# Kernel tuning notes

Hardware: AMD Instinct MI355X
Metric: run time of the kernel (lower is better)

## Reference

```python
import jax, jax.numpy as jnp
import numpy as np
import math

L, D, H, PK, N = 3, 512, 8, 8, 3072
DK = D // H


def _layernorm(x, s, b):
    m = jnp.mean(x, axis=-1, keepdims=True)
    v = jnp.mean((x - m) ** 2, axis=-1, keepdims=True)
    return (x - m) / jnp.sqrt(v + 1e-6) * s + b


def setup_inputs() -> dict:
    key = jax.random.key(0)
    ks = jax.random.split(key, 12)
    p = lambda k, shape: jax.random.normal(k, shape, jnp.float32) * (1.0 / math.sqrt(shape[-1]))
    x = jax.random.normal(ks[0], (N, D), jnp.float32)
    adm = jax.random.randint(ks[1], (N, N), 0, PK, jnp.int32)
    return {
        "x": x,
        "adm": adm,
        "ln_att_s": jnp.ones((L, D), jnp.float32),
        "ln_att_b": jnp.zeros((L, D), jnp.float32),
        "Wq": p(ks[2], (L, D, D)),
        "Wk": p(ks[3], (L, D, D)),
        "Wv": p(ks[4], (L, D, D)),
        "rel_k": p(ks[5], (L, PK, DK)),
        "Wg": p(ks[6], (L, D, D)) * 0.0,  # gating weight init to 0 in original
        "bg": jnp.ones((L, D), jnp.float32),  # gating bias init to 1
        "Wo": p(ks[7], (L, D, D)),
        "bo": jnp.zeros((L, D), jnp.float32),
        "ln_ff_s": jnp.ones((L, D), jnp.float32),
        "ln_ff_b": jnp.zeros((L, D), jnp.float32),
        "W1": p(ks[8], (L, D, 2 * D)),
        "b1": jnp.zeros((L, 2 * D), jnp.float32),
        "W2": p(ks[9], (L, 2 * D, D)),
        "b2": jnp.zeros((L, D), jnp.float32),
    }


def reference(x, adm, ln_att_s, ln_att_b, Wq, Wk, Wv, rel_k, Wg, bg, Wo, bo,
              ln_ff_s, ln_ff_b, W1, b1, W2, b2):
    att_scores = []
    idx = jnp.broadcast_to(adm[None], (H, N, N))  # one_hot(gpm) @ r  ==  gather r along PK
    for n in range(L):
        xn = _layernorm(x, ln_att_s[n], ln_att_b[n])  # same layer_norm applied to x_q and x_k
        q = (xn @ Wq[n]).reshape(N, H, DK).transpose(1, 0, 2)  # [H,N,DK]
        k = (xn @ Wk[n]).reshape(N, H, DK).transpose(1, 0, 2)
        v = (xn @ Wv[n]).reshape(N, H, DK).transpose(1, 0, 2)
        attn1 = jnp.einsum('hid,hjd->hij', q, k)  # [H,N,N]
        rq = jnp.einsum('hid,pd->hip', q, rel_k[n])  # [H,N,PK]
        attn2 = jnp.take_along_axis(rq, idx, axis=2)  # [H,N,N]
        attn = jax.nn.softmax((attn1 + attn2) / math.sqrt(DK), axis=-1)
        out = jnp.einsum('hij,hjd->hid', attn, v).transpose(1, 0, 2).reshape(N, D)
        gate = jax.nn.sigmoid(xn @ Wg[n] + bg[n])
        m = (out * gate) @ Wo[n] + bo[n]
        # FFN with pre-layernorm, residual: x = x + pff(x + m)
        y = x + m
        yn = _layernorm(y, ln_ff_s[n], ln_ff_b[n])
        ff = jax.nn.gelu(yn @ W1[n] + b1[n], approximate=True) @ W2[n] + b2[n]
        x = x + ff
        att_scores.append(attn)
    return (x, jnp.stack(att_scores))
```

## Files before the change

kernel.cpp:

```cpp
#include <hip/hip_runtime.h>
#include <math.h>

#define NT 3072
#define DIM 512
#define NH 8
#define DKH 64
#define PKN 8
#define D2 1024
#define NL 3

typedef float4 f4;
typedef unsigned short ushort_t;
typedef unsigned char uchar_t;
typedef __attribute__((ext_vector_type(8))) short s8x;
typedef __attribute__((ext_vector_type(4))) float fx4;

#define MFMA(a, b, c) __builtin_amdgcn_mfma_f32_16x16x32_bf16(a, b, c, 0, 0, 0)

__device__ __forceinline__ float b2f(ushort_t u) {
  union { unsigned int x; float f; } c;
  c.x = (unsigned int)u << 16;
  return c.f;
}
__device__ __forceinline__ ushort_t f2b(float f) {
  union { float f; unsigned int x; } c;
  c.f = f;
  unsigned int r = (c.x + 0x7FFFu + ((c.x >> 16) & 1u)) >> 16;
  return (ushort_t)r;
}

__device__ __forceinline__ float wred_sum(float v) {
#pragma unroll
  for (int off = 32; off > 0; off >>= 1) v += __shfl_xor(v, off);
  return v;
}

__global__ __launch_bounds__(256) void ln_bf16_kernel(
    const float* __restrict__ x, const float* __restrict__ s,
    const float* __restrict__ b, ushort_t* __restrict__ out) {
  int row = blockIdx.x;
  const float* xr = x + (size_t)row * DIM;
  int t = threadIdx.x;
  float v0 = xr[t], v1 = xr[t + 256];
  float sum = wred_sum(v0 + v1);
  float sq = wred_sum(v0 * v0 + v1 * v1);
  __shared__ float ss[4], s2[4];
  if ((t & 63) == 0) { ss[t >> 6] = sum; s2[t >> 6] = sq; }
  __syncthreads();
  float tot = ss[0] + ss[1] + ss[2] + ss[3];
  float tot2 = s2[0] + s2[1] + s2[2] + s2[3];
  float mean = tot * (1.0f / DIM);
  float var = tot2 * (1.0f / DIM) - mean * mean;
  float inv = rsqrtf(var + 1e-6f);
  ushort_t* orow = out + (size_t)row * DIM;
  orow[t] = f2b((v0 - mean) * inv * s[t] + b[t]);
  orow[t + 256] = f2b((v1 - mean) * inv * s[t + 256] + b[t + 256]);
}

__global__ __launch_bounds__(256) void tconv_kernel(const float* __restrict__ W,
                                                    ushort_t* __restrict__ Wt,
                                                    int K, int Nc) {
  __shared__ float Ls[64][65];
  int t = threadIdx.x;
  int n0 = blockIdx.x * 64, k0 = blockIdx.y * 64;
  int rr = t >> 4, cc = (t & 15) * 4;
#pragma unroll
  for (int p = 0; p < 4; ++p) {
    f4 v = *(const f4*)&W[(size_t)(k0 + rr + p * 16) * Nc + n0 + cc];
    Ls[rr + p * 16][cc + 0] = v.x;
    Ls[rr + p * 16][cc + 1] = v.y;
    Ls[rr + p * 16][cc + 2] = v.z;
    Ls[rr + p * 16][cc + 3] = v.w;
  }
  __syncthreads();
  int nr = t >> 2, kc = (t & 3) * 16;
  ushort_t tmp[16];
#pragma unroll
  for (int e = 0; e < 16; ++e) tmp[e] = f2b(Ls[kc + e][nr]);
  ushort_t* dst = &Wt[(size_t)(n0 + nr) * K + k0 + kc];
  *(uint4*)dst = *(uint4*)&tmp[0];
  *(uint4*)(dst + 8) = *(uint4*)&tmp[8];
}

__global__ __launch_bounds__(256) void adm8_kernel(const int* __restrict__ adm,
                                                   uchar_t* __restrict__ out) {
  size_t i = ((size_t)blockIdx.x * 256 + threadIdx.x) * 4;
  int4 v = *(const int4*)&adm[i];
  unsigned int b = (unsigned)(v.x & 255) | ((unsigned)(v.y & 255) << 8) |
                   ((unsigned)(v.z & 255) << 16) | ((unsigned)(v.w & 255) << 24);
  *(unsigned int*)&out[i] = b;
}

__global__ __launch_bounds__(64) void rq_kernel(const ushort_t* __restrict__ q,
                                                const float* __restrict__ relk,
                                                float* __restrict__ rq) {
  int i = blockIdx.x;
  int t = threadIdx.x;
  int h = t >> 3, p = t & 7;
  const ushort_t* qi = q + (size_t)i * DIM + h * DKH;
  const float* rp = relk + p * DKH;
  float s = 0.f;
#pragma unroll
  for (int d = 0; d < DKH; ++d) s = fmaf(b2f(qi[d]), rp[d], s);
  rq[(size_t)i * 64 + h * 8 + p] = s;
}

template <int ACT, bool OBF>
__global__ __launch_bounds__(256) void gemm_bf16(
    const ushort_t* __restrict__ A, const ushort_t* __restrict__ mul,
    const ushort_t* __restrict__ Bt, const float* __restrict__ bias,
    const float* __restrict__ res, void* __restrict__ Cp, int K, int ldc,
    float scale) {
  __shared__ __align__(16) ushort_t As[2048];
  __shared__ __align__(16) ushort_t Bs[2048];
  int t = threadIdx.x;
  int i0 = blockIdx.y * 64, j0 = blockIdx.x * 64;
  int w = t >> 6, l = t & 63;
  int wm = w >> 1, wn = w & 1;
  int lr = l >> 4, lc = l & 15;
  int fo = lr * 16 + (lc ^ (lr << 2));
  int am = t >> 2, akg = t & 3;
  int aoff = ((am >> 4) * 4 + akg) * 16 + ((am & 15) ^ (akg << 2));
  const ushort_t* Aptr = A + (size_t)(i0 + am) * K + akg * 8;
  const ushort_t* Mptr = mul ? mul + (size_t)(i0 + am) * K + akg * 8 : nullptr;
  int bc = l, bkg = w;
  int boff = ((bc >> 4) * 4 + bkg) * 16 + ((bc & 15) ^ (bkg << 2));
  const ushort_t* Bptr = Bt + (size_t)(j0 + bc) * K + bkg * 8;

  fx4 acc[2][2] = {};
  for (int k0 = 0; k0 < K; k0 += 32) {
    uint4 a = *(const uint4*)(Aptr + k0);
    if (mul) {
      uint4 m = *(const uint4*)(Mptr + k0);
      ushort_t* ap = (ushort_t*)&a;
      const ushort_t* mp = (const ushort_t*)&m;
#pragma unroll
      for (int e = 0; e < 8; ++e) ap[e] = f2b(b2f(ap[e]) * b2f(mp[e]));
    }
    *(uint4*)&As[aoff * 8] = a;
    *(uint4*)&Bs[boff * 8] = *(const uint4*)(Bptr + k0);
    __syncthreads();
    s8x a0 = *(const s8x*)&As[((wm * 2 + 0) * 64 + fo) * 8];
    s8x a1 = *(const s8x*)&As[((wm * 2 + 1) * 64 + fo) * 8];
    s8x b0 = *(const s8x*)&Bs[((wn * 2 + 0) * 64 + fo) * 8];
    s8x b1 = *(const s8x*)&Bs[((wn * 2 + 1) * 64 + fo) * 8];
    acc[0][0] = MFMA(a0, b0, acc[0][0]);
    acc[0][1] = MFMA(a0, b1, acc[0][1]);
    acc[1][0] = MFMA(a1, b0, acc[1][0]);
    acc[1][1] = MFMA(a1, b1, acc[1][1]);
    __syncthreads();
  }
#pragma unroll
  for (int ms = 0; ms < 2; ++ms) {
#pragma unroll
    for (int ns = 0; ns < 2; ++ns) {
#pragma unroll
      for (int r = 0; r < 4; ++r) {
        int i = i0 + (wm * 2 + ms) * 16 + lr * 4 + r;
        int j = j0 + (wn * 2 + ns) * 16 + lc;
        float o = acc[ms][ns][r] * scale;
        if (bias) o += bias[j];
        if (ACT == 1) {
          o = 1.0f / (1.0f + __expf(-o));
        } else if (ACT == 2) {
          float xx = o;
          float c = 0.7978845608028654f * (xx + 0.044715f * xx * xx * xx);
          o = 0.5f * xx * (1.0f + tanhf(c));
        }
        if (res) o += res[(size_t)i * ldc + j];
        if (OBF)
          ((ushort_t*)Cp)[(size_t)i * ldc + j] = f2b(o);
        else
          ((float*)Cp)[(size_t)i * ldc + j] = o;
      }
    }
  }
}

__global__ __launch_bounds__(256) void attn_kernel(
    const ushort_t* __restrict__ qb, const ushort_t* __restrict__ kb,
    const ushort_t* __restrict__ vb, const float* __restrict__ rqb,
    const uchar_t* __restrict__ adm8, float* __restrict__ att,
    ushort_t* __restrict__ av) {
  int h = blockIdx.y;
  int i0 = blockIdx.x * 64;
  __shared__ __align__(16) ushort_t Qs[4096];
  __shared__ __align__(16) ushort_t Ks[4096];
  __shared__ __align__(16) ushort_t Vs[4096];
  __shared__ __align__(16) ushort_t Ps[4096];
  __shared__ __align__(16) uchar_t adms[4096];
  __shared__ float rqs[64][8];
  int t = threadIdx.x, w = t >> 6, l = t & 63;
  int lr = l >> 4, lc = l & 15;
  int fo = lr * 16 + (lc ^ (lr << 2));
  {
    int am = t >> 2, akg = t & 3;
    int aoff = ((am >> 4) * 4 + akg) * 16 + ((am & 15) ^ (akg << 2));
    const ushort_t* qp = qb + (size_t)(i0 + am) * DIM + h * DKH + akg * 8;
    *(uint4*)&Qs[aoff * 8] = *(const uint4*)qp;
    *(uint4*)&Qs[2048 + aoff * 8] = *(const uint4*)(qp + 32);
  }
  if (t < 64) {
    const float* rp = &rqb[(size_t)(i0 + t) * 64 + h * 8];
    *(f4*)&rqs[t][0] = *(const f4*)rp;
    *(f4*)&rqs[t][4] = *(const f4*)(rp + 4);
  }
  __syncthreads();
  s8x qa0 = *(const s8x*)&Qs[(w * 64 + fo) * 8];
  s8x qa1 = *(const s8x*)&Qs[2048 + (w * 64 + fo) * 8];
  int bc = l, bkg = w;
  int boff = ((bc >> 4) * 4 + bkg) * 16 + ((bc & 15) ^ (bkg << 2));

  float m_run[4] = {-1e30f, -1e30f, -1e30f, -1e30f};
  float l_run[4] = {0.f, 0.f, 0.f, 0.f};

  for (int j0 = 0; j0 < NT; j0 += 64) {
    __syncthreads();
    const ushort_t* kp = kb + (size_t)(j0 + bc) * DIM + h * DKH + bkg * 8;
    *(uint4*)&Ks[boff * 8] = *(const uint4*)kp;
    *(uint4*)&Ks[2048 + boff * 8] = *(const uint4*)(kp + 32);
    *(uint4*)&adms[(t >> 2) * 64 + (t & 3) * 16] =
        *(const uint4*)&adm8[(size_t)(i0 + (t >> 2)) * NT + j0 + (t & 3) * 16];
    __syncthreads();
    fx4 sacc[4] = {};
#pragma unroll
    for (int nb = 0; nb < 4; ++nb) {
      s8x k0f = *(const s8x*)&Ks[(nb * 64 + fo) * 8];
      s8x k1f = *(const s8x*)&Ks[2048 + (nb * 64 + fo) * 8];
      sacc[nb] = MFMA(qa0, k0f, sacc[nb]);
      sacc[nb] = MFMA(qa1, k1f, sacc[nb]);
    }
#pragma unroll
    for (int r = 0; r < 4; ++r) {
      int il = w * 16 + lr * 4 + r;
      float sv[4];
      float tm = -1e30f;
#pragma unroll
      for (int nb = 0; nb < 4; ++nb) {
        sv[nb] = sacc[nb][r] + rqs[il][adms[il * 64 + nb * 16 + lc]];
        tm = fmaxf(tm, sv[nb]);
      }
      tm = fmaxf(tm, __shfl_xor(tm, 1));
      tm = fmaxf(tm, __shfl_xor(tm, 2));
      tm = fmaxf(tm, __shfl_xor(tm, 4));
      tm = fmaxf(tm, __shfl_xor(tm, 8));
      float mn = fmaxf(m_run[r], tm);
      float ssum = 0.f;
#pragma unroll
      for (int nb = 0; nb < 4; ++nb) ssum += __expf(sv[nb] - mn);
      ssum += __shfl_xor(ssum, 1);
      ssum += __shfl_xor(ssum, 2);
      ssum += __shfl_xor(ssum, 4);
      ssum += __shfl_xor(ssum, 8);
      l_run[r] = l_run[r] * __expf(m_run[r] - mn) + ssum;
      m_run[r] = mn;
    }
  }
  float linv[4];
#pragma unroll
  for (int r = 0; r < 4; ++r) linv[r] = 1.0f / l_run[r];

  fx4 oacc[4] = {};
  float* attb = att + ((size_t)h * NT + i0) * NT;
  for (int j0 = 0; j0 < NT; j0 += 64) {
    __syncthreads();
    const ushort_t* kp = kb + (size_t)(j0 + bc) * DIM + h * DKH + bkg * 8;
    *(uint4*)&Ks[boff * 8] = *(const uint4*)kp;
    *(uint4*)&Ks[2048 + boff * 8] = *(const uint4*)(kp + 32);
    *(uint4*)&adms[(t >> 2) * 64 + (t & 3) * 16] =
        *(const uint4*)&adm8[(size_t)(i0 + (t >> 2)) * NT + j0 + (t & 3) * 16];
#pragma unroll
    for (int cpass = 0; cpass < 2; ++cpass) {
      int cid = t + cpass * 256;
      int vks = cid >> 8, rem = cid & 255;
      int nb = rem >> 6, kg = (rem >> 4) & 3, s = rem & 15;
      const ushort_t* vp =
          vb + (size_t)(j0 + vks * 32 + kg * 8) * DIM + h * DKH + nb * 16 + s;
      ushort_t tmp[8];
#pragma unroll
      for (int e = 0; e < 8; ++e) tmp[e] = vp[(size_t)e * DIM];
      *(uint4*)&Vs[vks * 2048 + ((nb * 4 + kg) * 16 + (s ^ (kg << 2))) * 8] =
          *(uint4*)tmp;
    }
    __syncthreads();
    fx4 sacc[4] = {};
#pragma unroll
    for (int nb = 0; nb < 4; ++nb) {
      s8x k0f = *(const s8x*)&Ks[(nb * 64 + fo) * 8];
      s8x k1f = *(const s8x*)&Ks[2048 + (nb * 64 + fo) * 8];
      sacc[nb] = MFMA(qa0, k0f, sacc[nb]);
      sacc[nb] = MFMA(qa1, k1f, sacc[nb]);
    }
#pragma unroll
    for (int r = 0; r < 4; ++r) {
      int il = w * 16 + lr * 4 + r;
      int ir = il & 15;
#pragma unroll
      for (int nb = 0; nb < 4; ++nb) {
        int jl = nb * 16 + lc;
        float sval = sacc[nb][r] + rqs[il][adms[il * 64 + jl]];
        float p = __expf(sval - m_run[r]) * linv[r];
        attb[(size_t)il * NT + j0 + jl] = p;
        int pks = jl >> 5, pkg = (jl >> 3) & 3, pe = jl & 7;
        Ps[pks * 2048 + ((w * 4 + pkg) * 16 + (ir ^ (pkg << 2))) * 8 + pe] =
            f2b(p);
      }
    }
    __syncthreads();
#pragma unroll
    for (int ks = 0; ks < 2; ++ks) {
      s8x pa = *(const s8x*)&Ps[ks * 2048 + (w * 64 + fo) * 8];
#pragma unroll
      for (int nb = 0; nb < 4; ++nb) {
        s8x vf = *(const s8x*)&Vs[ks * 2048 + (nb * 64 + fo) * 8];
        oacc[nb] = MFMA(pa, vf, oacc[nb]);
      }
    }
  }
#pragma unroll
  for (int nb = 0; nb < 4; ++nb)
#pragma unroll
    for (int r = 0; r < 4; ++r)
      av[(size_t)(i0 + w * 16 + lr * 4 + r) * DIM + h * DKH + nb * 16 + lc] =
          f2b(oacc[nb][r]);
}

extern "C" void kernel_launch(void* const* d_in, const int* in_sizes, int n_in,
                              void* d_out, int out_size, void* d_ws,
                              size_t ws_size, hipStream_t stream) {
  const float* x_in = (const float*)d_in[0];
  const int* adm = (const int*)d_in[1];
  const float* ln_att_s = (const float*)d_in[2];
  const float* ln_att_b = (const float*)d_in[3];
  const float* Wq = (const float*)d_in[4];
  const float* Wk = (const float*)d_in[5];
  const float* Wv = (const float*)d_in[6];
  const float* rel_k = (const float*)d_in[7];
  const float* Wg = (const float*)d_in[8];
  const float* bg = (const float*)d_in[9];
  const float* Wo = (const float*)d_in[10];
  const float* bo = (const float*)d_in[11];
  const float* ln_ff_s = (const float*)d_in[12];
  const float* ln_ff_b = (const float*)d_in[13];
  const float* W1 = (const float*)d_in[14];
  const float* b1 = (const float*)d_in[15];
  const float* W2 = (const float*)d_in[16];
  const float* b2 = (const float*)d_in[17];
  float* out = (float*)d_out;

  const size_t ND = (size_t)NT * DIM;
  char* ws = (char*)d_ws;
  float* x_cur = (float*)ws;
  float* y = (float*)(ws + 6291456);
  ushort_t* qb = (ushort_t*)(ws + 12582912);
  ushort_t* kb = (ushort_t*)(ws + 15728640);
  ushort_t* vb = (ushort_t*)(ws + 18874368);
  ushort_t* gt = (ushort_t*)(ws + 22020096);
  ushort_t* avb = (ushort_t*)(ws + 25165824);
  ushort_t* xnb = (ushort_t*)(ws + 28311552);
  float* rqb = (float*)(ws + 31457280);
  uchar_t* adm8 = (uchar_t*)(ws + 32243712);
  ushort_t* Wt = (ushort_t*)(ws + 41680896);
  ushort_t* h1b = qb;

  ushort_t* Wtq = Wt;
  ushort_t* Wtk = Wt + 262144;
  ushort_t* Wtv = Wt + 524288;
  ushort_t* Wtg = Wt + 786432;
  ushort_t* Wto = Wt + 1048576;
  ushort_t* Wt1 = Wt + 1310720;
  ushort_t* Wt2 = Wt + 1835008;

  hipMemcpyAsync(x_cur, x_in, ND * sizeof(float), hipMemcpyDeviceToDevice,
                 stream);
  adm8_kernel<<<(NT * NT) / 1024, 256, 0, stream>>>(adm, adm8);

  dim3 gA(DIM / 64, NT / 64);
  dim3 gF1(D2 / 64, NT / 64);
  dim3 gT(8, 8);
  dim3 gT1(16, 8);
  dim3 gT2(8, 16);

  for (int n = 0; n < NL; ++n) {
    float* att = out + ND + (size_t)n * NH * NT * NT;
    size_t wo = (size_t)n * DIM * DIM;

    tconv_kernel<<<gT, 256, 0, stream>>>(Wq + wo, Wtq, DIM, DIM);
    tconv_kernel<<<gT, 256, 0, stream>>>(Wk + wo, Wtk, DIM, DIM);
    tconv_kernel<<<gT, 256, 0, stream>>>(Wv + wo, Wtv, DIM, DIM);
    tconv_kernel<<<gT, 256, 0, stream>>>(Wg + wo, Wtg, DIM, DIM);
    tconv_kernel<<<gT, 256, 0, stream>>>(Wo + wo, Wto, DIM, DIM);
    tconv_kernel<<<gT1, 256, 0, stream>>>(W1 + (size_t)n * DIM * D2, Wt1, DIM,
                                          D2);
    tconv_kernel<<<gT2, 256, 0, stream>>>(W2 + (size_t)n * D2 * DIM, Wt2, D2,
                                          DIM);

    ln_bf16_kernel<<<NT, 256, 0, stream>>>(x_cur, ln_att_s + n * DIM,
                                           ln_att_b + n * DIM, xnb);
    gemm_bf16<0, true><<<gA, 256, 0, stream>>>(xnb, nullptr, Wtq, nullptr,
                                               nullptr, qb, DIM, DIM, 0.125f);
    gemm_bf16<0, true><<<gA, 256, 0, stream>>>(xnb, nullptr, Wtk, nullptr,
                                               nullptr, kb, DIM, DIM, 1.0f);
    gemm_bf16<0, true><<<gA, 256, 0, stream>>>(xnb, nullptr, Wtv, nullptr,
                                               nullptr, vb, DIM, DIM, 1.0f);
    gemm_bf16<1, true><<<gA, 256, 0, stream>>>(xnb, nullptr, Wtg, bg + n * DIM,
                                               nullptr, gt, DIM, DIM, 1.0f);
    rq_kernel<<<NT, 64, 0, stream>>>(qb, rel_k + n * PKN * DKH, rqb);
    attn_kernel<<<dim3(NT / 64, NH), 256, 0, stream>>>(qb, kb, vb, rqb, adm8,
                                                       att, avb);
    gemm_bf16<0, false><<<gA, 256, 0, stream>>>(avb, gt, Wto, bo + n * DIM,
                                                x_cur, y, DIM, DIM, 1.0f);
    ln_bf16_kernel<<<NT, 256, 0, stream>>>(y, ln_ff_s + n * DIM,
                                           ln_ff_b + n * DIM, xnb);
    gemm_bf16<2, true><<<gF1, 256, 0, stream>>>(xnb, nullptr, Wt1, b1 + n * D2,
                                                nullptr, h1b, DIM, D2, 1.0f);
    gemm_bf16<0, false><<<gA, 256, 0, stream>>>(h1b, nullptr, Wt2, b2 + n * DIM,
                                                x_cur, x_cur, D2, DIM, 1.0f);
  }
  hipMemcpyAsync(out, x_cur, ND * sizeof(float), hipMemcpyDeviceToDevice,
                 stream);
}
```

Before: 1.199 ms.

## Fuse QKVG projections, restructure attention with split-KV waves and async LDS loads

```diff
diff --git a/kernel.cpp b/kernel.cpp
--- a/kernel.cpp
+++ b/kernel.cpp
@@ -8,6 +8,7 @@
 #define PKN 8
 #define D2 1024
 #define NL 3
+#define QS 2048
 
 typedef float4 f4;
 typedef unsigned short ushort_t;
@@ -16,6 +17,7 @@
 typedef __attribute__((ext_vector_type(4))) float fx4;
 
 #define MFMA(a, b, c) __builtin_amdgcn_mfma_f32_16x16x32_bf16(a, b, c, 0, 0, 0)
+#define EX2(x) __builtin_amdgcn_exp2f(x)
 
 __device__ __forceinline__ float b2f(ushort_t u) {
   union { unsigned int x; float f; } c;
@@ -28,11 +30,15 @@
   unsigned int r = (c.x + 0x7FFFu + ((c.x >> 16) & 1u)) >> 16;
   return (ushort_t)r;
 }
-
 __device__ __forceinline__ float wred_sum(float v) {
 #pragma unroll
   for (int off = 32; off > 0; off >>= 1) v += __shfl_xor(v, off);
   return v;
+}
+__device__ __forceinline__ void gload16(const ushort_t* g, ushort_t* l) {
+  __builtin_amdgcn_global_load_lds(
+      (const __attribute__((address_space(1))) unsigned int*)(const void*)g,
+      (__attribute__((address_space(3))) unsigned int*)(void*)l, 16, 0, 0);
 }
 
 __global__ __launch_bounds__(256) void ln_bf16_kernel(
@@ -57,12 +63,12 @@
   orow[t + 256] = f2b((v1 - mean) * inv * s[t + 256] + b[t + 256]);
 }
 
-__global__ __launch_bounds__(256) void tconv_kernel(const float* __restrict__ W,
-                                                    ushort_t* __restrict__ Wt,
-                                                    int K, int Nc) {
+__device__ __forceinline__ void tconv_body(const float* __restrict__ W,
+                                           ushort_t* __restrict__ Wt, int K,
+                                           int Nc, int tx, int ty) {
   __shared__ float Ls[64][65];
   int t = threadIdx.x;
-  int n0 = blockIdx.x * 64, k0 = blockIdx.y * 64;
+  int n0 = tx * 64, k0 = ty * 64;
   int rr = t >> 4, cc = (t & 15) * 4;
 #pragma unroll
   for (int p = 0; p < 4; ++p) {
@@ -80,6 +86,26 @@
   ushort_t* dst = &Wt[(size_t)(n0 + nr) * K + k0 + kc];
   *(uint4*)dst = *(uint4*)&tmp[0];
   *(uint4*)(dst + 8) = *(uint4*)&tmp[8];
+}
+
+__global__ __launch_bounds__(256) void wprep_kernel(
+    const float* __restrict__ Wq, const float* __restrict__ Wk,
+    const float* __restrict__ Wv, const float* __restrict__ Wg,
+    const float* __restrict__ Wo, const float* __restrict__ W1,
+    const float* __restrict__ W2, ushort_t* __restrict__ Wt) {
+  int bid = blockIdx.x;
+  if (bid < 320) {
+    int job = bid >> 6, tile = bid & 63;
+    const float* src = job == 0 ? Wq : job == 1 ? Wk : job == 2 ? Wv
+                       : job == 3 ? Wg : Wo;
+    tconv_body(src, Wt + (size_t)job * 262144, 512, 512, tile & 7, tile >> 3);
+  } else if (bid < 448) {
+    int tile = bid - 320;
+    tconv_body(W1, Wt + 1310720, 512, 1024, tile & 15, tile >> 4);
+  } else {
+    int tile = bid - 448;
+    tconv_body(W2, Wt + 1835008, 1024, 512, tile & 7, tile >> 3);
+  }
 }
 
 __global__ __launch_bounds__(256) void adm8_kernel(const int* __restrict__ adm,
@@ -91,23 +117,28 @@
   *(unsigned int*)&out[i] = b;
 }
 
-__global__ __launch_bounds__(64) void rq_kernel(const ushort_t* __restrict__ q,
-                                                const float* __restrict__ relk,
-                                                float* __restrict__ rq) {
-  int i = blockIdx.x;
+__global__ __launch_bounds__(256) void vt_kernel(const ushort_t* __restrict__ v,
+                                                 ushort_t* __restrict__ vbT) {
+  int jt = blockIdx.x, h = blockIdx.y;
+  __shared__ ushort_t L[64][72];
   int t = threadIdx.x;
-  int h = t >> 3, p = t & 7;
-  const ushort_t* qi = q + (size_t)i * DIM + h * DKH;
-  const float* rp = relk + p * DKH;
-  float s = 0.f;
-#pragma unroll
-  for (int d = 0; d < DKH; ++d) s = fmaf(b2f(qi[d]), rp[d], s);
-  rq[(size_t)i * 64 + h * 8 + p] = s;
+  int r = t >> 2, c = (t & 3) * 16;
+  const ushort_t* src = v + (size_t)(jt * 64 + r) * QS + h * 64 + c;
+  *(uint4*)&L[r][c] = *(const uint4*)src;
+  *(uint4*)&L[r][c + 8] = *(const uint4*)(src + 8);
+  __syncthreads();
+  int d = t >> 2, j0 = (t & 3) * 16;
+  ushort_t tmp[16];
+#pragma unroll
+  for (int e = 0; e < 16; ++e) tmp[e] = L[j0 + e][d];
+  ushort_t* dst = vbT + (size_t)(h * 64 + d) * NT + jt * 64 + j0;
+  *(uint4*)dst = *(uint4*)&tmp[0];
+  *(uint4*)(dst + 8) = *(uint4*)&tmp[8];
 }
 
 template <int ACT, bool OBF>
 __global__ __launch_bounds__(256) void gemm_bf16(
-    const ushort_t* __restrict__ A, const ushort_t* __restrict__ mul,
+    const ushort_t* __restrict__ A, const ushort_t* __restrict__ mul, int ldm,
     const ushort_t* __restrict__ Bt, const float* __restrict__ bias,
     const float* __restrict__ res, void* __restrict__ Cp, int K, int ldc,
     float scale) {
@@ -122,7 +153,7 @@
   int am = t >> 2, akg = t & 3;
   int aoff = ((am >> 4) * 4 + akg) * 16 + ((am & 15) ^ (akg << 2));
   const ushort_t* Aptr = A + (size_t)(i0 + am) * K + akg * 8;
-  const ushort_t* Mptr = mul ? mul + (size_t)(i0 + am) * K + akg * 8 : nullptr;
+  const ushort_t* Mptr = mul ? mul + (size_t)(i0 + am) * ldm + akg * 8 : nullptr;
   int bc = l, bkg = w;
   int boff = ((bc >> 4) * 4 + bkg) * 16 + ((bc & 15) ^ (bkg << 2));
   const ushort_t* Bptr = Bt + (size_t)(j0 + bc) * K + bkg * 8;
@@ -159,15 +190,23 @@
         int i = i0 + (wm * 2 + ms) * 16 + lr * 4 + r;
         int j = j0 + (wn * 2 + ns) * 16 + lc;
         float o = acc[ms][ns][r] * scale;
-        if (bias) o += bias[j];
-        if (ACT == 1) {
-          o = 1.0f / (1.0f + __expf(-o));
-        } else if (ACT == 2) {
-          float xx = o;
-          float c = 0.7978845608028654f * (xx + 0.044715f * xx * xx * xx);
-          o = 0.5f * xx * (1.0f + tanhf(c));
+        if (ACT == 3) {
+          if (blockIdx.x < 8) o *= 0.18033688011112042f;
+          if (blockIdx.x >= 24) {
+            o += bias[j & 511];
+            o = 1.0f / (1.0f + __expf(-o));
+          }
+        } else {
+          if (bias) o += bias[j];
+          if (ACT == 1) {
+            o = 1.0f / (1.0f + __expf(-o));
+          } else if (ACT == 2) {
+            float xx = o;
+            float c = 0.7978845608028654f * (xx + 0.044715f * xx * xx * xx);
+            o = 0.5f * xx * (1.0f + tanhf(c));
+          }
+          if (res) o += res[(size_t)i * ldc + j];
         }
-        if (res) o += res[(size_t)i * ldc + j];
         if (OBF)
           ((ushort_t*)Cp)[(size_t)i * ldc + j] = f2b(o);
         else
@@ -177,152 +216,236 @@
   }
 }
 
+__device__ __forceinline__ float rq_sel(const unsigned int* rqt,
+                                        unsigned int idx) {
+  unsigned int d01 = (idx & 2) ? rqt[1] : rqt[0];
+  unsigned int d23 = (idx & 2) ? rqt[3] : rqt[2];
+  unsigned int dd = (idx & 4) ? d23 : d01;
+  unsigned int r = (idx & 1) ? (dd & 0xffff0000u) : (dd << 16);
+  return __uint_as_float(r);
+}
+
 __global__ __launch_bounds__(256) void attn_kernel(
-    const ushort_t* __restrict__ qb, const ushort_t* __restrict__ kb,
-    const ushort_t* __restrict__ vb, const float* __restrict__ rqb,
-    const uchar_t* __restrict__ adm8, float* __restrict__ att,
-    ushort_t* __restrict__ av) {
+    const ushort_t* __restrict__ xqkvg, const ushort_t* __restrict__ vbT,
+    const float* __restrict__ relk, const uchar_t* __restrict__ adm8,
+    float* __restrict__ att, ushort_t* __restrict__ av) {
   int h = blockIdx.y;
-  int i0 = blockIdx.x * 64;
-  __shared__ __align__(16) ushort_t Qs[4096];
-  __shared__ __align__(16) ushort_t Ks[4096];
-  __shared__ __align__(16) ushort_t Vs[4096];
-  __shared__ __align__(16) ushort_t Ps[4096];
-  __shared__ __align__(16) uchar_t adms[4096];
-  __shared__ float rqs[64][8];
+  int i0 = blockIdx.x * 32;
   int t = threadIdx.x, w = t >> 6, l = t & 63;
   int lr = l >> 4, lc = l & 15;
-  int fo = lr * 16 + (lc ^ (lr << 2));
+  int ig = w & 1, jh = w >> 1;
+  int i_loc = ig * 16 + lc;
+  int i = i0 + i_loc;
+
+  __shared__ __align__(16) ushort_t Ks[2][4096];
+  __shared__ __align__(16) ushort_t Vs[2][4096];
+  __shared__ __align__(16) ushort_t Ps[2][2048];
+  __shared__ float Od[32][68];
+  __shared__ float MLs[2][2][16][2];
+
+  const ushort_t* qp = xqkvg + (size_t)i * QS + h * 64 + lr * 8;
+  s8x qf0 = *(const s8x*)qp;
+  s8x qf1 = *(const s8x*)(qp + 32);
+
+  unsigned int rqt[4];
   {
-    int am = t >> 2, akg = t & 3;
-    int aoff = ((am >> 4) * 4 + akg) * 16 + ((am & 15) ^ (akg << 2));
-    const ushort_t* qp = qb + (size_t)(i0 + am) * DIM + h * DKH + akg * 8;
-    *(uint4*)&Qs[aoff * 8] = *(const uint4*)qp;
-    *(uint4*)&Qs[2048 + aoff * 8] = *(const uint4*)(qp + 32);
-  }
-  if (t < 64) {
-    const float* rp = &rqb[(size_t)(i0 + t) * 64 + h * 8];
-    *(f4*)&rqs[t][0] = *(const f4*)rp;
-    *(f4*)&rqs[t][4] = *(const f4*)(rp + 4);
-  }
-  __syncthreads();
-  s8x qa0 = *(const s8x*)&Qs[(w * 64 + fo) * 8];
-  s8x qa1 = *(const s8x*)&Qs[2048 + (w * 64 + fo) * 8];
-  int bc = l, bkg = w;
-  int boff = ((bc >> 4) * 4 + bkg) * 16 + ((bc & 15) ^ (bkg << 2));
-
-  float m_run[4] = {-1e30f, -1e30f, -1e30f, -1e30f};
-  float l_run[4] = {0.f, 0.f, 0.f, 0.f};
-
-  for (int j0 = 0; j0 < NT; j0 += 64) {
-    __syncthreads();
-    const ushort_t* kp = kb + (size_t)(j0 + bc) * DIM + h * DKH + bkg * 8;
-    *(uint4*)&Ks[boff * 8] = *(const uint4*)kp;
-    *(uint4*)&Ks[2048 + boff * 8] = *(const uint4*)(kp + 32);
-    *(uint4*)&adms[(t >> 2) * 64 + (t & 3) * 16] =
-        *(const uint4*)&adm8[(size_t)(i0 + (t >> 2)) * NT + j0 + (t & 3) * 16];
-    __syncthreads();
-    fx4 sacc[4] = {};
-#pragma unroll
-    for (int nb = 0; nb < 4; ++nb) {
-      s8x k0f = *(const s8x*)&Ks[(nb * 64 + fo) * 8];
-      s8x k1f = *(const s8x*)&Ks[2048 + (nb * 64 + fo) * 8];
-      sacc[nb] = MFMA(qa0, k0f, sacc[nb]);
-      sacc[nb] = MFMA(qa1, k1f, sacc[nb]);
+    const ushort_t* q0 = (const ushort_t*)&qf0;
+    const ushort_t* q1 = (const ushort_t*)&qf1;
+    float sp[8];
+#pragma unroll
+    for (int p = 0; p < 8; ++p) {
+      const float* rp = relk + p * 64 + lr * 8;
+      float s = 0.f;
+#pragma unroll
+      for (int e = 0; e < 8; ++e) s = fmaf(b2f(q0[e]), rp[e], s);
+#pragma unroll
+      for (int e = 0; e < 8; ++e) s = fmaf(b2f(q1[e]), rp[32 + e], s);
+      s += __shfl_xor(s, 16);
+      s += __shfl_xor(s, 32);
+      sp[p] = s;
     }
 #pragma unroll
-    for (int r = 0; r < 4; ++r) {
-      int il = w * 16 + lr * 4 + r;
-      float sv[4];
+    for (int j = 0; j < 4; ++j)
+      rqt[j] = (unsigned int)f2b(sp[2 * j]) |
+               ((unsigned int)f2b(sp[2 * j + 1]) << 16);
+  }
+
+  int stgo = (w & 1) * 2048;
+  int srow = (w & 1) * 32 + (l >> 3);
+  int kp8 = ((l & 7) ^ (l >> 3)) * 8;
+  ushort_t* KS = Ks[jh];
+  ushort_t* VS = Vs[jh];
+  ushort_t* PS = Ps[jh];
+  const ushort_t* kSrc0 =
+      xqkvg + 512 + (size_t)(jh * 64 + srow) * QS + h * 64 + kp8;
+  const ushort_t* vSrc0 = vbT + (size_t)(h * 64 + srow) * NT + jh * 64 + kp8;
+  const uchar_t* admp0 = adm8 + (size_t)i * NT + jh * 64 + lr * 4;
+
+  int sw = (lc & 7);
+  int a_b0 = lc * 64 + ((lr ^ sw) << 3);
+  int a_b1 = lc * 64 + (((4 + lr) ^ sw) << 3);
+  int pb0 = i_loc * 64 + ((lr ^ sw) << 3);
+  int pb1 = i_loc * 64 + (((4 + lr) ^ sw) << 3);
+  int swz8 = sw << 3;
+
+  float m_run = -1e30f, l_run = 0.f;
+
+  {
+    const ushort_t* kSrc = kSrc0;
+    const uchar_t* admp = admp0;
+    for (int tt = 0; tt < 24; ++tt) {
+#pragma unroll
+      for (int q = 0; q < 4; ++q)
+        gload16(kSrc + (size_t)q * 8 * QS, KS + stgo + q * 512);
+      __syncthreads();
+      fx4 sacc[4] = {};
+#pragma unroll
+      for (int ja = 0; ja < 4; ++ja) {
+        s8x a0 = *(const s8x*)(KS + a_b0 + ja * 1024);
+        s8x a1 = *(const s8x*)(KS + a_b1 + ja * 1024);
+        sacc[ja] = MFMA(a0, qf0, sacc[ja]);
+        sacc[ja] = MFMA(a1, qf1, sacc[ja]);
+      }
+      float sv[4][4];
       float tm = -1e30f;
 #pragma unroll
-      for (int nb = 0; nb < 4; ++nb) {
-        sv[nb] = sacc[nb][r] + rqs[il][adms[il * 64 + nb * 16 + lc]];
-        tm = fmaxf(tm, sv[nb]);
-      }
-      tm = fmaxf(tm, __shfl_xor(tm, 1));
-      tm = fmaxf(tm, __shfl_xor(tm, 2));
-      tm = fmaxf(tm, __shfl_xor(tm, 4));
-      tm = fmaxf(tm, __shfl_xor(tm, 8));
-      float mn = fmaxf(m_run[r], tm);
-      float ssum = 0.f;
-#pragma unroll
-      for (int nb = 0; nb < 4; ++nb) ssum += __expf(sv[nb] - mn);
-      ssum += __shfl_xor(ssum, 1);
-      ssum += __shfl_xor(ssum, 2);
-      ssum += __shfl_xor(ssum, 4);
-      ssum += __shfl_xor(ssum, 8);
-      l_run[r] = l_run[r] * __expf(m_run[r] - mn) + ssum;
-      m_run[r] = mn;
+      for (int ja = 0; ja < 4; ++ja) {
+        unsigned int aw = *(const unsigned int*)(admp + ja * 16);
+#pragma unroll
+        for (int r = 0; r < 4; ++r) {
+          float vv = sacc[ja][r] + rq_sel(rqt, (aw >> (8 * r)) & 7u);
+          sv[ja][r] = vv;
+          tm = fmaxf(tm, vv);
+        }
+      }
+      float mn = fmaxf(m_run, tm);
+      float sum = 0.f;
+#pragma unroll
+      for (int ja = 0; ja < 4; ++ja)
+#pragma unroll
+        for (int r = 0; r < 4; ++r) sum += EX2(sv[ja][r] - mn);
+      l_run = l_run * EX2(m_run - mn) + sum;
+      m_run = mn;
+      kSrc += (size_t)128 * QS;
+      admp += 128;
+      __syncthreads();
     }
   }
-  float linv[4];
-#pragma unroll
-  for (int r = 0; r < 4; ++r) linv[r] = 1.0f / l_run[r];
+#pragma unroll
+  for (int off = 16; off <= 32; off <<= 1) {
+    float mo = __shfl_xor(m_run, off), lo = __shfl_xor(l_run, off);
+    float mn = fmaxf(m_run, mo);
+    l_run = l_run * EX2(m_run - mn) + lo * EX2(mo - mn);
+    m_run = mn;
+  }
+  if (l < 16) {
+    MLs[jh][ig][lc][0] = m_run;
+    MLs[jh][ig][lc][1] = l_run;
+  }
+  __syncthreads();
+  {
+    float mo = MLs[jh ^ 1][ig][lc][0], lo = MLs[jh ^ 1][ig][lc][1];
+    float mn = fmaxf(m_run, mo);
+    l_run = l_run * EX2(m_run - mn) + lo * EX2(mo - mn);
+    m_run = mn;
+  }
+  float lofs = m_run + __log2f(l_run);
+  __syncthreads();
 
   fx4 oacc[4] = {};
   float* attb = att + ((size_t)h * NT + i0) * NT;
-  for (int j0 = 0; j0 < NT; j0 += 64) {
-    __syncthreads();
-    const ushort_t* kp = kb + (size_t)(j0 + bc) * DIM + h * DKH + bkg * 8;
-    *(uint4*)&Ks[boff * 8] = *(const uint4*)kp;
-    *(uint4*)&Ks[2048 + boff * 8] = *(const uint4*)(kp + 32);
-    *(uint4*)&adms[(t >> 2) * 64 + (t & 3) * 16] =
-        *(const uint4*)&adm8[(size_t)(i0 + (t >> 2)) * NT + j0 + (t & 3) * 16];
-#pragma unroll
-    for (int cpass = 0; cpass < 2; ++cpass) {
-      int cid = t + cpass * 256;
-      int vks = cid >> 8, rem = cid & 255;
-      int nb = rem >> 6, kg = (rem >> 4) & 3, s = rem & 15;
-      const ushort_t* vp =
-          vb + (size_t)(j0 + vks * 32 + kg * 8) * DIM + h * DKH + nb * 16 + s;
-      ushort_t tmp[8];
-#pragma unroll
-      for (int e = 0; e < 8; ++e) tmp[e] = vp[(size_t)e * DIM];
-      *(uint4*)&Vs[vks * 2048 + ((nb * 4 + kg) * 16 + (s ^ (kg << 2))) * 8] =
-          *(uint4*)tmp;
+  int jh64 = jh * 64;
+  {
+    const ushort_t* kSrc = kSrc0;
+    const ushort_t* vSrc = vSrc0;
+    const uchar_t* admp = admp0;
+    for (int tt = 0; tt < 24; ++tt) {
+#pragma unroll
+      for (int q = 0; q < 4; ++q) {
+        gload16(kSrc + (size_t)q * 8 * QS, KS + stgo + q * 512);
+        gload16(vSrc + (size_t)q * 8 * NT, VS + stgo + q * 512);
+      }
+      __syncthreads();
+      fx4 sacc[4] = {};
+#pragma unroll
+      for (int ja = 0; ja < 4; ++ja) {
+        s8x a0 = *(const s8x*)(KS + a_b0 + ja * 1024);
+        s8x a1 = *(const s8x*)(KS + a_b1 + ja * 1024);
+        sacc[ja] = MFMA(a0, qf0, sacc[ja]);
+        sacc[ja] = MFMA(a1, qf1, sacc[ja]);
+      }
+#pragma unroll
+      for (int ja = 0; ja < 4; ++ja) {
+        unsigned int aw = *(const unsigned int*)(admp + ja * 16);
+        float p0 = EX2(sacc[ja][0] + rq_sel(rqt, aw & 7u) - lofs);
+        float p1 = EX2(sacc[ja][1] + rq_sel(rqt, (aw >> 8) & 7u) - lofs);
+        float p2 = EX2(sacc[ja][2] + rq_sel(rqt, (aw >> 16) & 7u) - lofs);
+        float p3 = EX2(sacc[ja][3] + rq_sel(rqt, (aw >> 24) & 7u) - lofs);
+        unsigned int w01 =
+            (unsigned int)f2b(p0) | ((unsigned int)f2b(p1) << 16);
+        unsigned int w23 =
+            (unsigned int)f2b(p2) | ((unsigned int)f2b(p3) << 16);
+        int cb = ja * 16 + lr * 4;
+        *(unsigned int*)&PS[i_loc * 64 + (cb ^ swz8)] = w01;
+        *(unsigned int*)&PS[i_loc * 64 + ((cb + 2) ^ swz8)] = w23;
+      }
+      __syncthreads();
+#pragma unroll
+      for (int ks = 0; ks < 2; ++ks) {
+        s8x pf = *(const s8x*)(PS + (ks == 0 ? pb0 : pb1));
+#pragma unroll
+        for (int nd = 0; nd < 4; ++nd) {
+          s8x vf = *(const s8x*)(VS + (ks == 0 ? a_b0 : a_b1) + nd * 1024);
+          oacc[nd] = MFMA(vf, pf, oacc[nd]);
+        }
+      }
+      {
+        int uu = (w & 1) * 64 + l;
+        int row = uu >> 2, cs = (uu & 3) * 16;
+        int rsw = (row & 7) << 3;
+        uint4 A_ = *(const uint4*)&PS[row * 64 + (cs ^ rsw)];
+        uint4 B_ = *(const uint4*)&PS[row * 64 + ((cs + 8) ^ rsw)];
+        const ushort_t* ap = (const ushort_t*)&A_;
+        const ushort_t* bp = (const ushort_t*)&B_;
+        float* op = attb + (size_t)row * NT + tt * 128 + jh64 + cs;
+        f4 o0 = {b2f(ap[0]), b2f(ap[1]), b2f(ap[2]), b2f(ap[3])};
+        f4 o1 = {b2f(ap[4]), b2f(ap[5]), b2f(ap[6]), b2f(ap[7])};
+        f4 o2 = {b2f(bp[0]), b2f(bp[1]), b2f(bp[2]), b2f(bp[3])};
+        f4 o3 = {b2f(bp[4]), b2f(bp[5]), b2f(bp[6]), b2f(bp[7])};
+        *(f4*)(op + 0) = o0;
+        *(f4*)(op + 4) = o1;
+        *(f4*)(op + 8) = o2;
+        *(f4*)(op + 12) = o3;
+      }
+      kSrc += (size_t)128 * QS;
+      vSrc += 128;
+      admp += 128;
+      __syncthreads();
     }
-    __syncthreads();
-    fx4 sacc[4] = {};
-#pragma unroll
-    for (int nb = 0; nb < 4; ++nb) {
-      s8x k0f = *(const s8x*)&Ks[(nb * 64 + fo) * 8];
-      s8x k1f = *(const s8x*)&Ks[2048 + (nb * 64 + fo) * 8];
-      sacc[nb] = MFMA(qa0, k0f, sacc[nb]);
-      sacc[nb] = MFMA(qa1, k1f, sacc[nb]);
-    }
-#pragma unroll
-    for (int r = 0; r < 4; ++r) {
-      int il = w * 16 + lr * 4 + r;
-      int ir = il & 15;
-#pragma unroll
-      for (int nb = 0; nb < 4; ++nb) {
-        int jl = nb * 16 + lc;
-        float sval = sacc[nb][r] + rqs[il][adms[il * 64 + jl]];
-        float p = __expf(sval - m_run[r]) * linv[r];
-        attb[(size_t)il * NT + j0 + jl] = p;
-        int pks = jl >> 5, pkg = (jl >> 3) & 3, pe = jl & 7;
-        Ps[pks * 2048 + ((w * 4 + pkg) * 16 + (ir ^ (pkg << 2))) * 8 + pe] =
-            f2b(p);
-      }
-    }
-    __syncthreads();
-#pragma unroll
-    for (int ks = 0; ks < 2; ++ks) {
-      s8x pa = *(const s8x*)&Ps[ks * 2048 + (w * 64 + fo) * 8];
-#pragma unroll
-      for (int nb = 0; nb < 4; ++nb) {
-        s8x vf = *(const s8x*)&Vs[ks * 2048 + (nb * 64 + fo) * 8];
-        oacc[nb] = MFMA(pa, vf, oacc[nb]);
-      }
-    }
-  }
-#pragma unroll
-  for (int nb = 0; nb < 4; ++nb)
-#pragma unroll
-    for (int r = 0; r < 4; ++r)
-      av[(size_t)(i0 + w * 16 + lr * 4 + r) * DIM + h * DKH + nb * 16 + lc] =
-          f2b(oacc[nb][r]);
+  }
+  if (jh == 1) {
+#pragma unroll
+    for (int nd = 0; nd < 4; ++nd)
+#pragma unroll
+      for (int r = 0; r < 4; ++r) Od[i_loc][nd * 16 + lr * 4 + r] = oacc[nd][r];
+  }
+  __syncthreads();
+  if (jh == 0) {
+#pragma unroll
+    for (int nd = 0; nd < 4; ++nd)
+#pragma unroll
+      for (int r = 0; r < 4; ++r)
+        Od[i_loc][nd * 16 + lr * 4 + r] += oacc[nd][r];
+  }
+  __syncthreads();
+  {
+    int row = t >> 3, ds = (t & 7) * 8;
+    f4 oA = *(const f4*)&Od[row][ds];
+    f4 oB = *(const f4*)&Od[row][ds + 4];
+    ushort_t tmp[8] = {f2b(oA.x), f2b(oA.y), f2b(oA.z), f2b(oA.w),
+                       f2b(oB.x), f2b(oB.y), f2b(oB.z), f2b(oB.w)};
+    *(uint4*)&av[(size_t)(i0 + row) * DIM + h * 64 + ds] = *(uint4*)tmp;
+  }
 }
 
 extern "C" void kernel_launch(void* const* d_in, const int* in_sizes, int n_in,
@@ -352,70 +475,47 @@
   char* ws = (char*)d_ws;
   float* x_cur = (float*)ws;
   float* y = (float*)(ws + 6291456);
-  ushort_t* qb = (ushort_t*)(ws + 12582912);
-  ushort_t* kb = (ushort_t*)(ws + 15728640);
-  ushort_t* vb = (ushort_t*)(ws + 18874368);
-  ushort_t* gt = (ushort_t*)(ws + 22020096);
+  ushort_t* xqkvg = (ushort_t*)(ws + 12582912);
   ushort_t* avb = (ushort_t*)(ws + 25165824);
   ushort_t* xnb = (ushort_t*)(ws + 28311552);
-  float* rqb = (float*)(ws + 31457280);
-  uchar_t* adm8 = (uchar_t*)(ws + 32243712);
-  ushort_t* Wt = (ushort_t*)(ws + 41680896);
-  ushort_t* h1b = qb;
-
-  ushort_t* Wtq = Wt;
-  ushort_t* Wtk = Wt + 262144;
-  ushort_t* Wtv = Wt + 524288;
-  ushort_t* Wtg = Wt + 786432;
-  ushort_t* Wto = Wt + 1048576;
-  ushort_t* Wt1 = Wt + 1310720;
-  ushort_t* Wt2 = Wt + 1835008;
+  ushort_t* vbT = (ushort_t*)(ws + 31457280);
+  uchar_t* adm8 = (uchar_t*)(ws + 34603008);
+  ushort_t* Wt = (ushort_t*)(ws + 44040192);
+  ushort_t* h1b = xqkvg;
 
   hipMemcpyAsync(x_cur, x_in, ND * sizeof(float), hipMemcpyDeviceToDevice,
                  stream);
   adm8_kernel<<<(NT * NT) / 1024, 256, 0, stream>>>(adm, adm8);
 
-  dim3 gA(DIM / 64, NT / 64);
-  dim3 gF1(D2 / 64, NT / 64);
-  dim3 gT(8, 8);
-  dim3 gT1(16, 8);
-  dim3 gT2(8, 16);
+  dim3 gQKVG(32, NT / 64);
+  dim3 gA(8, NT / 64);
+  dim3 gF1(16, NT / 64);
 
   for (int n = 0; n < NL; ++n) {
     float* att = out + ND + (size_t)n * NH * NT * NT;
     size_t wo = (size_t)n * DIM * DIM;
 
-    tconv_kernel<<<gT, 256, 0, stream>>>(Wq + wo, Wtq, DIM, DIM);
-    tconv_kernel<<<gT, 256, 0, stream>>>(Wk + wo, Wtk, DIM, DIM);
-    tconv_kernel<<<gT, 256, 0, stream>>>(Wv + wo, Wtv, DIM, DIM);
-    tconv_kernel<<<gT, 256, 0, stream>>>(Wg + wo, Wtg, DIM, DIM);
-    tconv_kernel<<<gT, 256, 0, stream>>>(Wo + wo, Wto, DIM, DIM);
-    tconv_kernel<<<gT1, 256, 0, stream>>>(W1 + (size_t)n * DIM * D2, Wt1, DIM,
-                                          D2);
-    tconv_kernel<<<gT2, 256, 0, stream>>>(W2 + (size_t)n * D2 * DIM, Wt2, D2,
-                                          DIM);
-
+    wprep_kernel<<<576, 256, 0, stream>>>(Wq + wo, Wk + wo, Wv + wo, Wg + wo,
+                                          Wo + wo, W1 + (size_t)n * DIM * D2,
+                                          W2 + (size_t)n * D2 * DIM, Wt);
     ln_bf16_kernel<<<NT, 256, 0, stream>>>(x_cur, ln_att_s + n * DIM,
                                            ln_att_b + n * DIM, xnb);
-    gemm_bf16<0, true><<<gA, 256, 0, stream>>>(xnb, nullptr, Wtq, nullptr,
-                                               nullptr, qb, DIM, DIM, 0.125f);
-    gemm_bf16<0, true><<<gA, 256, 0, stream>>>(xnb, nullptr, Wtk, nullptr,
-                                               nullptr, kb, DIM, DIM, 1.0f);
-    gemm_bf16<0, true><<<gA, 256, 0, stream>>>(xnb, nullptr, Wtv, nullptr,
-                                               nullptr, vb, DIM, DIM, 1.0f);
-    gemm_bf16<1, true><<<gA, 256, 0, stream>>>(xnb, nullptr, Wtg, bg + n * DIM,
-                                               nullptr, gt, DIM, DIM, 1.0f);
-    rq_kernel<<<NT, 64, 0, stream>>>(qb, rel_k + n * PKN * DKH, rqb);
-    attn_kernel<<<dim3(NT / 64, NH), 256, 0, stream>>>(qb, kb, vb, rqb, adm8,
-                                                       att, avb);
-    gemm_bf16<0, false><<<gA, 256, 0, stream>>>(avb, gt, Wto, bo + n * DIM,
-                                                x_cur, y, DIM, DIM, 1.0f);
+    gemm_bf16<3, true><<<gQKVG, 256, 0, stream>>>(
+        xnb, nullptr, 0, Wt, bg + n * DIM, nullptr, xqkvg, DIM, QS, 1.0f);
+    vt_kernel<<<dim3(NT / 64, NH), 256, 0, stream>>>(xqkvg + 1024, vbT);
+    attn_kernel<<<dim3(NT / 32, NH), 256, 0, stream>>>(
+        xqkvg, vbT, rel_k + n * PKN * DKH, adm8, att, avb);
+    gemm_bf16<0, false><<<gA, 256, 0, stream>>>(
+        avb, xqkvg + 1536, QS, Wt + 1048576, bo + n * DIM, x_cur, y, DIM, DIM,
+        1.0f);
     ln_bf16_kernel<<<NT, 256, 0, stream>>>(y, ln_ff_s + n * DIM,
                                            ln_ff_b + n * DIM, xnb);
-    gemm_bf16<2, true><<<gF1, 256, 0, stream>>>(xnb, nullptr, Wt1, b1 + n * D2,
-                                                nullptr, h1b, DIM, D2, 1.0f);
-    gemm_bf16<0, false><<<gA, 256, 0, stream>>>(h1b, nullptr, Wt2, b2 + n * DIM,
-                                                x_cur, x_cur, D2, DIM, 1.0f);
+    gemm_bf16<2, true><<<gF1, 256, 0, stream>>>(xnb, nullptr, 0, Wt + 1310720,
+                                                b1 + n * D2, nullptr, h1b, DIM,
+                                                D2, 1.0f);
+    gemm_bf16<0, false><<<gA, 256, 0, stream>>>(h1b, nullptr, 0, Wt + 1835008,
+                                                b2 + n * DIM, x_cur, x_cur, D2,
+                                                DIM, 1.0f);
   }
   hipMemcpyAsync(out, x_cur, ND * sizeof(float), hipMemcpyDeviceToDevice,
                  stream);
```

Result: faster. 1.137 ms (-5.2%).
